# Kernel tuning notes

Measured on AMD Instinct MI355X. Metric: run time of the kernel, lower is better.

Reference implementation:

```python
import jax, jax.numpy as jnp
import numpy as np

EPS = 1e-06
NUM_HEADS = 16
HEAD_DIM = 72
HIDDEN = 1152
N = 4096


def _rms_norm(x, weight=None):
    # x: [..., head_dim]; computed in fp32 as in the torch reference
    xf = x.astype(jnp.float32)
    ms = jnp.mean(xf * xf, axis=-1, keepdims=True) + EPS
    y = xf * jax.lax.rsqrt(ms)
    if weight is not None:
        y = y * weight.astype(jnp.float32)
    return y.astype(x.dtype)


def _rotate_half(x):
    h = x.shape[-1] // 2
    return jnp.concatenate([-x[..., h:], x[..., :h]], axis=-1)


def _apply_2d_rope(x, cos, sin):
    # x: [n, H, head_dim]; cos/sin: [n, head_dim] (first half dim-0 freqs, second half dim-1)
    hd = x.shape[-1]
    x1, x2 = x[..., : hd // 2], x[..., hd // 2 :]
    c1, c2 = jnp.split(cos, 2, axis=-1)
    s1, s2 = jnp.split(sin, 2, axis=-1)

    def ap(xp, c, s):
        c = c[:, None, :]  # broadcast over heads (unsqueeze_dim=1)
        s = s[:, None, :]
        return xp * c + _rotate_half(xp) * s

    return jnp.concatenate([ap(x1, c1, s1), ap(x2, c2, s2)], axis=-1)


def setup_inputs() -> dict:
    key = jax.random.key(0)
    ks = jax.random.split(key, 8)
    hidden_states = jax.random.normal(ks[0], (N, HIDDEN), dtype=jnp.float32)
    cos = jax.random.uniform(ks[1], (N, HEAD_DIM), dtype=jnp.float32, minval=-1.0, maxval=1.0)
    sin = jax.random.uniform(ks[2], (N, HEAD_DIM), dtype=jnp.float32, minval=-1.0, maxval=1.0)
    proj = NUM_HEADS * HEAD_DIM
    Wq = jax.random.normal(ks[3], (HIDDEN, proj), dtype=jnp.float32) * 0.02
    Wk = jax.random.normal(ks[4], (HIDDEN, proj), dtype=jnp.float32) * 0.02
    Wv = jax.random.normal(ks[5], (HIDDEN, proj), dtype=jnp.float32) * 0.02
    Wo = jax.random.normal(ks[6], (proj, HIDDEN), dtype=jnp.float32) * 0.02
    q_scale = jnp.ones((HEAD_DIM,), dtype=jnp.float32)
    k_scale = jnp.ones((HEAD_DIM,), dtype=jnp.float32)
    return {
        "hidden_states": hidden_states, "cos": cos, "sin": sin,
        "Wq": Wq, "Wk": Wk, "Wv": Wv, "Wo": Wo,
        "q_scale": q_scale, "k_scale": k_scale,
    }


def reference(hidden_states, cos, sin, Wq, Wk, Wv, Wo, q_scale, k_scale):
    n = hidden_states.shape[0]
    xq = (hidden_states @ Wq).reshape(n, NUM_HEADS, HEAD_DIM)
    xk = (hidden_states @ Wk).reshape(n, NUM_HEADS, HEAD_DIM)
    xv = (hidden_states @ Wv).reshape(n, NUM_HEADS, HEAD_DIM)
    xq = _rms_norm(xq, q_scale)
    xk = _rms_norm(xk, k_scale)
    xv = _rms_norm(xv)  # no scale
    xq = _apply_2d_rope(xq, cos, sin)
    xk = _apply_2d_rope(xk, cos, sin)
    # eager bidirectional attention, scale = 1.0
    attn = jnp.einsum("nhd,mhd->hnm", xq, xk)  # [H, n, n]
    attn = jax.nn.softmax(attn.astype(jnp.float32), axis=-1).astype(xq.dtype)
    out = jnp.einsum("hnm,mhd->nhd", attn, xv)  # [n, H, d]
    out = out.reshape(n, NUM_HEADS * HEAD_DIM)
    return out @ Wo
```

## Files before the change

### kernel.cpp

```cpp
#include <hip/hip_runtime.h>
#include <stdint.h>

typedef unsigned short u16;
typedef __bf16 bf16x8 __attribute__((ext_vector_type(8)));
typedef float f32x4 __attribute__((ext_vector_type(4)));
typedef __attribute__((address_space(1))) const unsigned int as1_u32;
typedef __attribute__((address_space(3))) unsigned int as3_u32;

#define SEQ 4096
#define HID 1152
#define NH 16
#define HD 72

__device__ __forceinline__ void gload_lds16(const void* g, void* l) {
  __builtin_amdgcn_global_load_lds((as1_u32*)g, (as3_u32*)l, 16, 0, 0);
}
__device__ __forceinline__ u16 f2bf(float f) {
  __bf16 h = (__bf16)f;
  return __builtin_bit_cast(u16, h);
}
__device__ __forceinline__ float bf2f(u16 u) {
  unsigned int x = ((unsigned int)u) << 16;
  return __builtin_bit_cast(float, x);
}

__global__ void cvt_x(const float* __restrict__ X, u16* __restrict__ Xb, int n4) {
  int i = blockIdx.x * blockDim.x + threadIdx.x;
  if (i < n4) {
    float4 v = *(const float4*)(X + (size_t)i * 4);
    unsigned int lo = f2bf(v.x) | ((unsigned int)f2bf(v.y) << 16);
    unsigned int hi = f2bf(v.z) | ((unsigned int)f2bf(v.w) << 16);
    *(uint2*)(Xb + (size_t)i * 4) = make_uint2(lo, hi);
  }
}

__global__ void transpose_w(const float* __restrict__ Wq, const float* __restrict__ Wk,
                            const float* __restrict__ Wv, const float* __restrict__ Wo,
                            u16* __restrict__ Wt, u16* __restrict__ Wot) {
  __shared__ __align__(16) float t[32][33];
  int z = blockIdx.z;
  const float* src = (z == 0) ? Wq : (z == 1) ? Wk : (z == 2) ? Wv : Wo;
  u16* dst = (z < 3) ? (Wt + (size_t)z * HID * HID) : Wot;
  int tx = threadIdx.x & 31, ty = threadIdx.x >> 5;
  int c0 = blockIdx.x * 32, r0 = blockIdx.y * 32;
#pragma unroll
  for (int i = 0; i < 4; i++)
    t[ty + i * 8][tx] = src[(size_t)(r0 + ty + i * 8) * HID + c0 + tx];
  __syncthreads();
#pragma unroll
  for (int i = 0; i < 4; i++)
    dst[(size_t)(c0 + ty + i * 8) * HID + r0 + tx] = f2bf(t[tx][ty + i * 8]);
}

template <int OUTBF16>
__global__ __launch_bounds__(256, 2) void gemm_bt(const u16* __restrict__ A,
                                                  const u16* __restrict__ Bt,
                                                  void* __restrict__ Cout,
                                                  int M, int N, int K) {
  __shared__ __align__(16) u16 lds[2][2][128 * 64];
  const int tid = threadIdx.x;
  const int wave = tid >> 6, lane = tid & 63;
  const int l15 = lane & 15, l4 = lane >> 4;
  const size_t bm = (size_t)blockIdx.x * 128, bn = (size_t)blockIdx.y * 128;
  const int wm = (wave >> 1) * 64, wn = (wave & 1) * 64;
  const int nt = K >> 6;

  f32x4 acc[4][4] = {};

  auto stage = [&](int buf, int kt) {
    const int k0 = kt << 6;
#pragma unroll
    for (int r = 0; r < 4; r++) {
      int idx = (r << 8) + tid;
      int m = idx >> 3, j = idx & 7;
      int js = j ^ (m & 7);
      void* ldsA = (void*)&lds[buf][0][(size_t)((r << 8) + (wave << 6)) * 8];
      void* ldsB = (void*)&lds[buf][1][(size_t)((r << 8) + (wave << 6)) * 8];
      gload_lds16(A + (bm + m) * (size_t)K + k0 + js * 8, ldsA);
      gload_lds16(Bt + (bn + m) * (size_t)K + k0 + js * 8, ldsB);
    }
  };

  stage(0, 0);
  for (int t = 0; t < nt; t++) {
    __syncthreads();
    if (t + 1 < nt) stage((t + 1) & 1, t + 1);
    const u16* As = &lds[t & 1][0][0];
    const u16* Bs = &lds[t & 1][1][0];
#pragma unroll
    for (int kk = 0; kk < 2; kk++) {
      bf16x8 af[4], bfr[4];
      int slot = (kk << 2) + l4;
#pragma unroll
      for (int mi = 0; mi < 4; mi++) {
        int m = wm + (mi << 4) + l15;
        af[mi] = *(const bf16x8*)&As[m * 64 + ((slot ^ (m & 7)) << 3)];
      }
#pragma unroll
      for (int ni = 0; ni < 4; ni++) {
        int n = wn + (ni << 4) + l15;
        bfr[ni] = *(const bf16x8*)&Bs[n * 64 + ((slot ^ (n & 7)) << 3)];
      }
#pragma unroll
      for (int mi = 0; mi < 4; mi++)
#pragma unroll
        for (int ni = 0; ni < 4; ni++)
          acc[mi][ni] = __builtin_amdgcn_mfma_f32_16x16x32_bf16(af[mi], bfr[ni], acc[mi][ni], 0, 0, 0);
    }
  }

#pragma unroll
  for (int mi = 0; mi < 4; mi++)
#pragma unroll
    for (int ni = 0; ni < 4; ni++)
#pragma unroll
      for (int r = 0; r < 4; r++) {
        size_t m = bm + wm + (mi << 4) + (l4 << 2) + r;
        size_t n = bn + wn + (ni << 4) + l15;
        if (OUTBF16)
          ((u16*)Cout)[m * N + n] = f2bf(acc[mi][ni][r]);
        else
          ((float*)Cout)[m * N + n] = acc[mi][ni][r];
      }
}

__global__ __launch_bounds__(256, 2) void norm_rope(
    const u16* __restrict__ C1, const float* __restrict__ cosv,
    const float* __restrict__ sinv, const float* __restrict__ qsc,
    const float* __restrict__ ksc, u16* __restrict__ Qp, u16* __restrict__ Kp,
    u16* __restrict__ Vt) {
  __shared__ __align__(16) u16 in_t[32 * 224];
  __shared__ __align__(16) u16 qo[32 * 128];
  __shared__ __align__(16) u16 ko[32 * 128];
  __shared__ __align__(16) u16 vo[80 * 48];
  const int tid = threadIdx.x;
  const int h = blockIdx.y;
  const int n0 = blockIdx.x * 32;

#pragma unroll
  for (int k = 0; k < 4; k++) {
    int g = tid + k * 256;
    if (g < 864) {
      int row = g / 27, j = g - row * 27;
      int seg = j / 9, c = (j - seg * 9) * 8;
      const u16* src = C1 + (size_t)(n0 + row) * 3456 + seg * 1152 + h * HD + c;
      *(uint4*)&in_t[row * 224 + j * 8] = *(const uint4*)src;
    }
  }
  __syncthreads();

  const int r = tid >> 3, p = tid & 7;
  float sq = 0, sk = 0, sv = 0;
  auto acc8 = [&](int off, float& s) {
    uint4 v = *(const uint4*)&in_t[r * 224 + off];
    unsigned int vv[4] = {v.x, v.y, v.z, v.w};
#pragma unroll
    for (int q = 0; q < 4; q++) {
      float a = bf2f((u16)(vv[q] & 0xffff));
      float b = bf2f((u16)(vv[q] >> 16));
      s += a * a + b * b;
    }
  };
  acc8(0 + p * 8, sq);
  acc8(72 + p * 8, sk);
  acc8(144 + p * 8, sv);
  if (p == 0) { acc8(64, sq); acc8(136, sk); acc8(208, sv); }
#pragma unroll
  for (int m = 1; m < 8; m <<= 1) {
    sq += __shfl_xor(sq, m);
    sk += __shfl_xor(sk, m);
    sv += __shfl_xor(sv, m);
  }
  const float rq = rsqrtf(sq * (1.0f / 72.0f) + 1e-6f);
  const float rk = rsqrtf(sk * (1.0f / 72.0f) + 1e-6f);
  const float rv = rsqrtf(sv * (1.0f / 72.0f) + 1e-6f);

#pragma unroll
  for (int u = 0; u < 5; u++) {
    int ti = p + (u << 3);
    if (ti < 36) {
      int i1 = ti + ((ti >= 18) ? 18 : 0);
      int i2 = i1 + 18;
      const float* cb = cosv + (size_t)(n0 + r) * HD;
      const float* sb = sinv + (size_t)(n0 + r) * HD;
      float c1 = cb[i1], c2 = cb[i2], s1 = sb[i1], s2 = sb[i2];
      float q1 = bf2f(in_t[r * 224 + i1]) * rq * qsc[i1];
      float q2 = bf2f(in_t[r * 224 + i2]) * rq * qsc[i2];
      float k1 = bf2f(in_t[r * 224 + 72 + i1]) * rk * ksc[i1];
      float k2 = bf2f(in_t[r * 224 + 72 + i2]) * rk * ksc[i2];
      qo[r * 128 + i1] = f2bf(q1 * c1 - q2 * s1);
      qo[r * 128 + i2] = f2bf(q2 * c2 + q1 * s2);
      ko[r * 128 + i1] = f2bf(k1 * c1 - k2 * s1);
      ko[r * 128 + i2] = f2bf(k2 * c2 + k1 * s2);
    }
  }
#pragma unroll
  for (int u = 0; u < 9; u++) {
    int d = p * 9 + u;
    vo[d * 48 + r] = f2bf(bf2f(in_t[r * 224 + 144 + d]) * rv);
  }
  if (p < 7) {
    uint4 z = make_uint4(0, 0, 0, 0);
    *(uint4*)&qo[r * 128 + (9 + p) * 8] = z;
    *(uint4*)&ko[r * 128 + (9 + p) * 8] = z;
  }
  if (tid < 32) {
    int d = 72 + (tid >> 2), g = tid & 3;
    *(uint4*)&vo[d * 48 + g * 8] = make_uint4(0, 0, 0, 0);
  }
  __syncthreads();

#pragma unroll
  for (int k = 0; k < 2; k++) {
    int g = tid + k * 256;
    int row = g >> 4, j = g & 15;
    *(uint4*)(Qp + ((size_t)h * SEQ + n0 + row) * 128 + j * 8) = *(const uint4*)&qo[row * 128 + j * 8];
    *(uint4*)(Kp + ((size_t)h * SEQ + n0 + row) * 128 + j * 8) = *(const uint4*)&ko[row * 128 + j * 8];
  }
#pragma unroll
  for (int k = 0; k < 2; k++) {
    int g = tid + k * 256;
    if (g < 320) {
      int d = g >> 2, j = g & 3;
      *(uint4*)(Vt + ((size_t)h * 80 + d) * SEQ + n0 + j * 8) = *(const uint4*)&vo[d * 48 + j * 8];
    }
  }
}

__global__ __launch_bounds__(256, 2) void attn(const u16* __restrict__ Qp,
                                               const u16* __restrict__ Kp,
                                               const u16* __restrict__ Vt,
                                               u16* __restrict__ AO) {
  __shared__ __align__(16) u16 Ks[2][64 * 128];
  __shared__ __align__(16) u16 Vs[2][80 * 64];
  __shared__ __align__(16) u16 Ps[4][32 * 64];
  const int tid = threadIdx.x;
  const int wave = tid >> 6, lane = tid & 63;
  const int l15 = lane & 15, l4 = lane >> 4;
  const int h = blockIdx.y;
  const int q0 = blockIdx.x * 128 + wave * 32;

  bf16x8 bq[2][3];
#pragma unroll
  for (int qf = 0; qf < 2; qf++) {
    const u16* qbase = Qp + ((size_t)h * SEQ + q0 + qf * 16 + l15) * 128;
#pragma unroll
    for (int kk = 0; kk < 3; kk++) bq[qf][kk] = *(const bf16x8*)(qbase + kk * 32 + l4 * 8);
  }

  f32x4 acc[2][5] = {};
  float mi_[2] = {-1e30f, -1e30f};
  float li_[2] = {0.0f, 0.0f};

  auto stage = [&](int buf, int k0) {
#pragma unroll
    for (int rr = 0; rr < 4; rr++) {
      int g = (rr << 8) + tid;
      int m = g >> 4, j = g & 15;
      int js = j ^ (m & 15);
      gload_lds16(Kp + ((size_t)h * SEQ + k0 + m) * 128 + js * 8,
                  (void*)&Ks[buf][(size_t)((rr << 8) + (wave << 6)) * 8]);
    }
#pragma unroll
    for (int rr = 0; rr < 3; rr++) {
      int c = (rr << 2) + wave;
      if (c < 10) {
        int g = (c << 6) + lane;
        int d = g >> 3, j = g & 7;
        int js = j ^ (d & 7);
        gload_lds16(Vt + ((size_t)h * 80 + d) * SEQ + k0 + js * 8,
                    (void*)&Vs[buf][(size_t)(c << 6) * 8]);
      }
    }
  };

  stage(0, 0);
  for (int t = 0; t < 64; t++) {
    __syncthreads();
    if (t < 63) stage((t + 1) & 1, (t + 1) * 64);
    const u16* Kb = Ks[t & 1];
    const u16* Vb = Vs[t & 1];

    f32x4 s[2][4] = {};
#pragma unroll
    for (int kk = 0; kk < 3; kk++) {
      int slot = (kk << 2) + l4;
      bf16x8 ak[4];
#pragma unroll
      for (int nf = 0; nf < 4; nf++) {
        int row = (nf << 4) + l15;
        ak[nf] = *(const bf16x8*)&Kb[row * 128 + ((slot ^ (row & 15)) << 3)];
      }
#pragma unroll
      for (int qf = 0; qf < 2; qf++)
#pragma unroll
        for (int nf = 0; nf < 4; nf++)
          s[qf][nf] = __builtin_amdgcn_mfma_f32_16x16x32_bf16(ak[nf], bq[qf][kk], s[qf][nf], 0, 0, 0);
    }

    float scl[2];
#pragma unroll
    for (int qf = 0; qf < 2; qf++) {
      float v0 = fmaxf(fmaxf(s[qf][0][0], s[qf][0][1]), fmaxf(s[qf][0][2], s[qf][0][3]));
      float v1 = fmaxf(fmaxf(s[qf][1][0], s[qf][1][1]), fmaxf(s[qf][1][2], s[qf][1][3]));
      float v2 = fmaxf(fmaxf(s[qf][2][0], s[qf][2][1]), fmaxf(s[qf][2][2], s[qf][2][3]));
      float v3 = fmaxf(fmaxf(s[qf][3][0], s[qf][3][1]), fmaxf(s[qf][3][2], s[qf][3][3]));
      float v = fmaxf(fmaxf(v0, v1), fmaxf(v2, v3));
      v = fmaxf(v, __shfl_xor(v, 16));
      v = fmaxf(v, __shfl_xor(v, 32));
      float mnew = fmaxf(mi_[qf], v);
      scl[qf] = __expf(mi_[qf] - mnew);
      mi_[qf] = mnew;
      float rsum = 0.0f;
      int row = (qf << 4) + l15;
#pragma unroll
      for (int nf = 0; nf < 4; nf++) {
        ushort4 pk;
        float p0 = __expf(s[qf][nf][0] - mnew);
        float p1 = __expf(s[qf][nf][1] - mnew);
        float p2 = __expf(s[qf][nf][2] - mnew);
        float p3 = __expf(s[qf][nf][3] - mnew);
        rsum += (p0 + p1) + (p2 + p3);
        pk.x = f2bf(p0); pk.y = f2bf(p1); pk.z = f2bf(p2); pk.w = f2bf(p3);
        int gg = (nf << 2) + l4;
        int gs = gg ^ ((row & 7) << 1);
        *(ushort4*)&Ps[wave][row * 64 + gs * 4] = pk;
      }
      rsum += __shfl_xor(rsum, 16);
      rsum += __shfl_xor(rsum, 32);
      li_[qf] = li_[qf] * scl[qf] + rsum;
    }

#pragma unroll
    for (int qf = 0; qf < 2; qf++)
#pragma unroll
      for (int r = 0; r < 4; r++) {
        float sr = __shfl(scl[qf], (l4 << 2) + r);
#pragma unroll
        for (int ni = 0; ni < 5; ni++) acc[qf][ni][r] *= sr;
      }

#pragma unroll
    for (int kk = 0; kk < 2; kk++) {
      bf16x8 pa[2];
#pragma unroll
      for (int qf = 0; qf < 2; qf++) {
        int row = (qf << 4) + l15;
        int gb = ((kk << 3) + (l4 << 1)) ^ ((row & 7) << 1);
        pa[qf] = *(const bf16x8*)&Ps[wave][row * 64 + gb * 4];
      }
      int slot = (kk << 2) + l4;
#pragma unroll
      for (int ni = 0; ni < 5; ni++) {
        int d = (ni << 4) + l15;
        bf16x8 bv = *(const bf16x8*)&Vb[d * 64 + ((slot ^ (d & 7)) << 3)];
#pragma unroll
        for (int qf = 0; qf < 2; qf++)
          acc[qf][ni] = __builtin_amdgcn_mfma_f32_16x16x32_bf16(pa[qf], bv, acc[qf][ni], 0, 0, 0);
      }
    }
  }

#pragma unroll
  for (int qf = 0; qf < 2; qf++)
#pragma unroll
    for (int r = 0; r < 4; r++) {
      float inv = 1.0f / __shfl(li_[qf], (l4 << 2) + r);
      int q = q0 + (qf << 4) + (l4 << 2) + r;
#pragma unroll
      for (int ni = 0; ni < 5; ni++) {
        int d = (ni << 4) + l15;
        if (d < HD) AO[(size_t)q * HID + h * HD + d] = f2bf(acc[qf][ni][r] * inv);
      }
    }
}

extern "C" void kernel_launch(void* const* d_in, const int* in_sizes, int n_in,
                              void* d_out, int out_size, void* d_ws, size_t ws_size,
                              hipStream_t stream) {
  const float* X = (const float*)d_in[0];
  const float* cosv = (const float*)d_in[1];
  const float* sinv = (const float*)d_in[2];
  const float* Wq = (const float*)d_in[3];
  const float* Wk = (const float*)d_in[4];
  const float* Wv = (const float*)d_in[5];
  const float* Wo = (const float*)d_in[6];
  const float* qsc = (const float*)d_in[7];
  const float* ksc = (const float*)d_in[8];
  float* out = (float*)d_out;

  uint8_t* ws = (uint8_t*)d_ws;
  u16* Xb  = (u16*)(ws);
  u16* Wt  = (u16*)(ws + 9437184);
  u16* Wot = (u16*)(ws + 17399808);
  u16* C1  = (u16*)(ws + 20054016);
  u16* Qp  = (u16*)(ws + 48365568);
  u16* Kp  = (u16*)(ws + 65142784);
  u16* Vt  = (u16*)(ws + 81920000);
  u16* AO  = Xb;

  cvt_x<<<4608, 256, 0, stream>>>(X, Xb, (SEQ * HID) / 4);
  transpose_w<<<dim3(36, 36, 4), 256, 0, stream>>>(Wq, Wk, Wv, Wo, Wt, Wot);
  gemm_bt<1><<<dim3(32, 27), 256, 0, stream>>>(Xb, Wt, (void*)C1, SEQ, 3456, HID);
  norm_rope<<<dim3(128, 16), 256, 0, stream>>>(C1, cosv, sinv, qsc, ksc, Qp, Kp, Vt);
  attn<<<dim3(32, 16), 256, 0, stream>>>(Qp, Kp, Vt, AO);
  gemm_bt<0><<<dim3(32, 9), 256, 0, stream>>>(AO, Wot, (void*)out, SEQ, HID, HID);
}
```

Baseline: 343.8 us.

## Shrink Q/K padding to 96 and use 8-wave attention blocks

Q and K rows are now padded to 96 instead of 128 elements, which shrinks the global staging buffers and the K tile in shared memory and removes the XOR swizzle on K. The attention kernel now runs 512 threads with 16 query rows per wave instead of 32, and remaps block IDs so heads are interleaved across blocks. It also adds s_setprio around the MFMA sections and defers the row-sum cross-lane reduction to the end. The aim is less memory traffic and padding work plus more waves to hide latency, at the cost of less K/V reuse per wave and possible LDS bank conflicts from the unswizzled K reads.

```diff
diff --git a/kernel.cpp b/kernel.cpp
--- a/kernel.cpp
+++ b/kernel.cpp
@@ -130,8 +130,8 @@
     const float* __restrict__ ksc, u16* __restrict__ Qp, u16* __restrict__ Kp,
     u16* __restrict__ Vt) {
   __shared__ __align__(16) u16 in_t[32 * 224];
-  __shared__ __align__(16) u16 qo[32 * 128];
-  __shared__ __align__(16) u16 ko[32 * 128];
+  __shared__ __align__(16) u16 qo[32 * 96];
+  __shared__ __align__(16) u16 ko[32 * 96];
   __shared__ __align__(16) u16 vo[80 * 48];
   const int tid = threadIdx.x;
   const int h = blockIdx.y;
@@ -188,10 +188,10 @@
       float q2 = bf2f(in_t[r * 224 + i2]) * rq * qsc[i2];
       float k1 = bf2f(in_t[r * 224 + 72 + i1]) * rk * ksc[i1];
       float k2 = bf2f(in_t[r * 224 + 72 + i2]) * rk * ksc[i2];
-      qo[r * 128 + i1] = f2bf(q1 * c1 - q2 * s1);
-      qo[r * 128 + i2] = f2bf(q2 * c2 + q1 * s2);
-      ko[r * 128 + i1] = f2bf(k1 * c1 - k2 * s1);
-      ko[r * 128 + i2] = f2bf(k2 * c2 + k1 * s2);
+      qo[r * 96 + i1] = f2bf(q1 * c1 - q2 * s1);
+      qo[r * 96 + i2] = f2bf(q2 * c2 + q1 * s2);
+      ko[r * 96 + i1] = f2bf(k1 * c1 - k2 * s1);
+      ko[r * 96 + i2] = f2bf(k2 * c2 + k1 * s2);
     }
   }
 #pragma unroll
@@ -199,10 +199,10 @@
     int d = p * 9 + u;
     vo[d * 48 + r] = f2bf(bf2f(in_t[r * 224 + 144 + d]) * rv);
   }
-  if (p < 7) {
+  if (p < 3) {
     uint4 z = make_uint4(0, 0, 0, 0);
-    *(uint4*)&qo[r * 128 + (9 + p) * 8] = z;
-    *(uint4*)&ko[r * 128 + (9 + p) * 8] = z;
+    *(uint4*)&qo[r * 96 + (9 + p) * 8] = z;
+    *(uint4*)&ko[r * 96 + (9 + p) * 8] = z;
   }
   if (tid < 32) {
     int d = 72 + (tid >> 2), g = tid & 3;
@@ -213,9 +213,11 @@
 #pragma unroll
   for (int k = 0; k < 2; k++) {
     int g = tid + k * 256;
-    int row = g >> 4, j = g & 15;
-    *(uint4*)(Qp + ((size_t)h * SEQ + n0 + row) * 128 + j * 8) = *(const uint4*)&qo[row * 128 + j * 8];
-    *(uint4*)(Kp + ((size_t)h * SEQ + n0 + row) * 128 + j * 8) = *(const uint4*)&ko[row * 128 + j * 8];
+    if (g < 384) {
+      int row = g / 12, j = g - row * 12;
+      *(uint4*)(Qp + ((size_t)h * SEQ + n0 + row) * 96 + j * 8) = *(const uint4*)&qo[row * 96 + j * 8];
+      *(uint4*)(Kp + ((size_t)h * SEQ + n0 + row) * 96 + j * 8) = *(const uint4*)&ko[row * 96 + j * 8];
+    }
   }
 #pragma unroll
   for (int k = 0; k < 2; k++) {
@@ -227,49 +229,54 @@
   }
 }
 
-__global__ __launch_bounds__(256, 2) void attn(const u16* __restrict__ Qp,
+__global__ __launch_bounds__(512, 4) void attn(const u16* __restrict__ Qp,
                                                const u16* __restrict__ Kp,
                                                const u16* __restrict__ Vt,
                                                u16* __restrict__ AO) {
-  __shared__ __align__(16) u16 Ks[2][64 * 128];
+  __shared__ __align__(16) u16 Ks[2][64 * 96];
   __shared__ __align__(16) u16 Vs[2][80 * 64];
-  __shared__ __align__(16) u16 Ps[4][32 * 64];
+  __shared__ __align__(16) u16 Ps[8][16 * 64];
   const int tid = threadIdx.x;
   const int wave = tid >> 6, lane = tid & 63;
   const int l15 = lane & 15, l4 = lane >> 4;
-  const int h = blockIdx.y;
-  const int q0 = blockIdx.x * 128 + wave * 32;
-
-  bf16x8 bq[2][3];
-#pragma unroll
-  for (int qf = 0; qf < 2; qf++) {
-    const u16* qbase = Qp + ((size_t)h * SEQ + q0 + qf * 16 + l15) * 128;
-#pragma unroll
-    for (int kk = 0; kk < 3; kk++) bq[qf][kk] = *(const bf16x8*)(qbase + kk * 32 + l4 * 8);
-  }
-
-  f32x4 acc[2][5] = {};
-  float mi_[2] = {-1e30f, -1e30f};
-  float li_[2] = {0.0f, 0.0f};
+
+  const int bid = blockIdx.x + (blockIdx.y << 5);
+  const int h = ((bid & 7) << 1) | ((bid >> 3) & 1);
+  const int qt = bid >> 4;
+  const int q0 = qt * 128 + wave * 16;
+
+  bf16x8 bq[3];
+  const u16* qbase = Qp + ((size_t)h * SEQ + q0 + l15) * 96;
+#pragma unroll
+  for (int kk = 0; kk < 3; kk++) bq[kk] = *(const bf16x8*)(qbase + kk * 32 + l4 * 8);
+
+  f32x4 acc[5] = {};
+  float mi_ = -1e30f, li_ = 0.0f;
 
   auto stage = [&](int buf, int k0) {
-#pragma unroll
-    for (int rr = 0; rr < 4; rr++) {
-      int g = (rr << 8) + tid;
-      int m = g >> 4, j = g & 15;
-      int js = j ^ (m & 15);
-      gload_lds16(Kp + ((size_t)h * SEQ + k0 + m) * 128 + js * 8,
-                  (void*)&Ks[buf][(size_t)((rr << 8) + (wave << 6)) * 8]);
-    }
-#pragma unroll
-    for (int rr = 0; rr < 3; rr++) {
-      int c = (rr << 2) + wave;
-      if (c < 10) {
-        int g = (c << 6) + lane;
-        int d = g >> 3, j = g & 7;
-        int js = j ^ (d & 7);
-        gload_lds16(Vt + ((size_t)h * 80 + d) * SEQ + k0 + js * 8,
-                    (void*)&Vs[buf][(size_t)(c << 6) * 8]);
+    {
+      int g = tid;
+      int m = g / 12, j = g - m * 12;
+      gload_lds16(Kp + ((size_t)h * SEQ + k0 + m) * 96 + j * 8,
+                  (void*)&Ks[buf][(size_t)(wave << 6) * 8]);
+      if (wave < 4) {
+        int g2 = tid + 512;
+        int m2 = g2 / 12, j2 = g2 - m2 * 12;
+        gload_lds16(Kp + ((size_t)h * SEQ + k0 + m2) * 96 + j2 * 8,
+                    (void*)&Ks[buf][(size_t)(512 + (wave << 6)) * 8]);
+      }
+    }
+    {
+      int d = tid >> 3, j = tid & 7;
+      int js = j ^ (d & 7);
+      gload_lds16(Vt + ((size_t)h * 80 + d) * SEQ + k0 + js * 8,
+                  (void*)&Vs[buf][(size_t)(wave << 6) * 8]);
+      if (wave < 2) {
+        int g2 = tid + 512;
+        int d2 = g2 >> 3, j2 = g2 & 7;
+        int js2 = j2 ^ (d2 & 7);
+        gload_lds16(Vt + ((size_t)h * 80 + d2) * SEQ + k0 + js2 * 8,
+                    (void*)&Vs[buf][(size_t)(512 + (wave << 6)) * 8]);
       }
     }
   };
@@ -281,7 +288,8 @@
     const u16* Kb = Ks[t & 1];
     const u16* Vb = Vs[t & 1];
 
-    f32x4 s[2][4] = {};
+    f32x4 s[4] = {};
+    __builtin_amdgcn_s_setprio(1);
 #pragma unroll
     for (int kk = 0; kk < 3; kk++) {
       int slot = (kk << 2) + l4;
@@ -289,90 +297,74 @@
 #pragma unroll
       for (int nf = 0; nf < 4; nf++) {
         int row = (nf << 4) + l15;
-        ak[nf] = *(const bf16x8*)&Kb[row * 128 + ((slot ^ (row & 15)) << 3)];
-      }
-#pragma unroll
-      for (int qf = 0; qf < 2; qf++)
-#pragma unroll
-        for (int nf = 0; nf < 4; nf++)
-          s[qf][nf] = __builtin_amdgcn_mfma_f32_16x16x32_bf16(ak[nf], bq[qf][kk], s[qf][nf], 0, 0, 0);
-    }
-
-    float scl[2];
-#pragma unroll
-    for (int qf = 0; qf < 2; qf++) {
-      float v0 = fmaxf(fmaxf(s[qf][0][0], s[qf][0][1]), fmaxf(s[qf][0][2], s[qf][0][3]));
-      float v1 = fmaxf(fmaxf(s[qf][1][0], s[qf][1][1]), fmaxf(s[qf][1][2], s[qf][1][3]));
-      float v2 = fmaxf(fmaxf(s[qf][2][0], s[qf][2][1]), fmaxf(s[qf][2][2], s[qf][2][3]));
-      float v3 = fmaxf(fmaxf(s[qf][3][0], s[qf][3][1]), fmaxf(s[qf][3][2], s[qf][3][3]));
-      float v = fmaxf(fmaxf(v0, v1), fmaxf(v2, v3));
-      v = fmaxf(v, __shfl_xor(v, 16));
-      v = fmaxf(v, __shfl_xor(v, 32));
-      float mnew = fmaxf(mi_[qf], v);
-      scl[qf] = __expf(mi_[qf] - mnew);
-      mi_[qf] = mnew;
-      float rsum = 0.0f;
-      int row = (qf << 4) + l15;
-#pragma unroll
-      for (int nf = 0; nf < 4; nf++) {
-        ushort4 pk;
-        float p0 = __expf(s[qf][nf][0] - mnew);
-        float p1 = __expf(s[qf][nf][1] - mnew);
-        float p2 = __expf(s[qf][nf][2] - mnew);
-        float p3 = __expf(s[qf][nf][3] - mnew);
-        rsum += (p0 + p1) + (p2 + p3);
-        pk.x = f2bf(p0); pk.y = f2bf(p1); pk.z = f2bf(p2); pk.w = f2bf(p3);
-        int gg = (nf << 2) + l4;
-        int gs = gg ^ ((row & 7) << 1);
-        *(ushort4*)&Ps[wave][row * 64 + gs * 4] = pk;
-      }
-      rsum += __shfl_xor(rsum, 16);
-      rsum += __shfl_xor(rsum, 32);
-      li_[qf] = li_[qf] * scl[qf] + rsum;
-    }
-
-#pragma unroll
-    for (int qf = 0; qf < 2; qf++)
-#pragma unroll
-      for (int r = 0; r < 4; r++) {
-        float sr = __shfl(scl[qf], (l4 << 2) + r);
-#pragma unroll
-        for (int ni = 0; ni < 5; ni++) acc[qf][ni][r] *= sr;
-      }
-
+        ak[nf] = *(const bf16x8*)&Kb[row * 96 + slot * 8];
+      }
+#pragma unroll
+      for (int nf = 0; nf < 4; nf++)
+        s[nf] = __builtin_amdgcn_mfma_f32_16x16x32_bf16(ak[nf], bq[kk], s[nf], 0, 0, 0);
+    }
+    __builtin_amdgcn_s_setprio(0);
+
+    float v0 = fmaxf(fmaxf(s[0][0], s[0][1]), fmaxf(s[0][2], s[0][3]));
+    float v1 = fmaxf(fmaxf(s[1][0], s[1][1]), fmaxf(s[1][2], s[1][3]));
+    float v2 = fmaxf(fmaxf(s[2][0], s[2][1]), fmaxf(s[2][2], s[2][3]));
+    float v3 = fmaxf(fmaxf(s[3][0], s[3][1]), fmaxf(s[3][2], s[3][3]));
+    float v = fmaxf(fmaxf(v0, v1), fmaxf(v2, v3));
+    v = fmaxf(v, __shfl_xor(v, 16));
+    v = fmaxf(v, __shfl_xor(v, 32));
+    float mnew = fmaxf(mi_, v);
+    float scl = __expf(mi_ - mnew);
+    mi_ = mnew;
+    float rsum = 0.0f;
+#pragma unroll
+    for (int nf = 0; nf < 4; nf++) {
+      ushort4 pk;
+      float p0 = __expf(s[nf][0] - mnew);
+      float p1 = __expf(s[nf][1] - mnew);
+      float p2 = __expf(s[nf][2] - mnew);
+      float p3 = __expf(s[nf][3] - mnew);
+      rsum += (p0 + p1) + (p2 + p3);
+      pk.x = f2bf(p0); pk.y = f2bf(p1); pk.z = f2bf(p2); pk.w = f2bf(p3);
+      int gs = ((nf << 2) + l4) ^ ((l15 & 7) << 1);
+      *(ushort4*)&Ps[wave][l15 * 64 + gs * 4] = pk;
+    }
+    li_ = li_ * scl + rsum;
+
+#pragma unroll
+    for (int r = 0; r < 4; r++) {
+      float sr = __shfl(scl, (l4 << 2) + r);
+#pragma unroll
+      for (int ni = 0; ni < 5; ni++) acc[ni][r] *= sr;
+    }
+
+    __builtin_amdgcn_s_setprio(1);
 #pragma unroll
     for (int kk = 0; kk < 2; kk++) {
-      bf16x8 pa[2];
-#pragma unroll
-      for (int qf = 0; qf < 2; qf++) {
-        int row = (qf << 4) + l15;
-        int gb = ((kk << 3) + (l4 << 1)) ^ ((row & 7) << 1);
-        pa[qf] = *(const bf16x8*)&Ps[wave][row * 64 + gb * 4];
-      }
+      int gb = ((kk << 3) + (l4 << 1)) ^ ((l15 & 7) << 1);
+      bf16x8 pa = *(const bf16x8*)&Ps[wave][l15 * 64 + gb * 4];
       int slot = (kk << 2) + l4;
 #pragma unroll
       for (int ni = 0; ni < 5; ni++) {
         int d = (ni << 4) + l15;
         bf16x8 bv = *(const bf16x8*)&Vb[d * 64 + ((slot ^ (d & 7)) << 3)];
-#pragma unroll
-        for (int qf = 0; qf < 2; qf++)
-          acc[qf][ni] = __builtin_amdgcn_mfma_f32_16x16x32_bf16(pa[qf], bv, acc[qf][ni], 0, 0, 0);
-      }
-    }
-  }
-
-#pragma unroll
-  for (int qf = 0; qf < 2; qf++)
-#pragma unroll
-    for (int r = 0; r < 4; r++) {
-      float inv = 1.0f / __shfl(li_[qf], (l4 << 2) + r);
-      int q = q0 + (qf << 4) + (l4 << 2) + r;
-#pragma unroll
-      for (int ni = 0; ni < 5; ni++) {
-        int d = (ni << 4) + l15;
-        if (d < HD) AO[(size_t)q * HID + h * HD + d] = f2bf(acc[qf][ni][r] * inv);
-      }
-    }
+        acc[ni] = __builtin_amdgcn_mfma_f32_16x16x32_bf16(pa, bv, acc[ni], 0, 0, 0);
+      }
+    }
+    __builtin_amdgcn_s_setprio(0);
+  }
+
+  li_ += __shfl_xor(li_, 16);
+  li_ += __shfl_xor(li_, 32);
+#pragma unroll
+  for (int r = 0; r < 4; r++) {
+    float inv = 1.0f / __shfl(li_, (l4 << 2) + r);
+    int q = q0 + (l4 << 2) + r;
+#pragma unroll
+    for (int ni = 0; ni < 5; ni++) {
+      int d = (ni << 4) + l15;
+      if (d < HD) AO[(size_t)q * HID + h * HD + d] = f2bf(acc[ni][r] * inv);
+    }
+  }
 }
 
 extern "C" void kernel_launch(void* const* d_in, const int* in_sizes, int n_in,
@@ -395,14 +387,14 @@
   u16* Wot = (u16*)(ws + 17399808);
   u16* C1  = (u16*)(ws + 20054016);
   u16* Qp  = (u16*)(ws + 48365568);
-  u16* Kp  = (u16*)(ws + 65142784);
-  u16* Vt  = (u16*)(ws + 81920000);
+  u16* Kp  = (u16*)(ws + 60948480);
+  u16* Vt  = (u16*)(ws + 73531392);
   u16* AO  = Xb;
 
   cvt_x<<<4608, 256, 0, stream>>>(X, Xb, (SEQ * HID) / 4);
   transpose_w<<<dim3(36, 36, 4), 256, 0, stream>>>(Wq, Wk, Wv, Wo, Wt, Wot);
   gemm_bt<1><<<dim3(32, 27), 256, 0, stream>>>(Xb, Wt, (void*)C1, SEQ, 3456, HID);
   norm_rope<<<dim3(128, 16), 256, 0, stream>>>(C1, cosv, sinv, qsc, ksc, Qp, Kp, Vt);
-  attn<<<dim3(32, 16), 256, 0, stream>>>(Qp, Kp, Vt, AO);
+  attn<<<dim3(32, 16), 512, 0, stream>>>(Qp, Kp, Vt, AO);
   gemm_bt<0><<<dim3(32, 9), 256, 0, stream>>>(AO, Wot, (void*)out, SEQ, HID, HID);
 }
```

Result: faster. 307.6 us (-10.5%).
